# Performance work log

Measured on AMD Instinct MI355X. Metric: run time of the kernel, lower is better.

## Reference

```python
import jax, jax.numpy as jnp
import numpy as np

N = 100000   # nodes
E = 1600000  # edges
D = 128      # feature dim
DO = 3       # out_head target dim
C = 50000    # centers


def setup_inputs() -> dict:
    key = jax.random.key(0)
    k1, k2, k3, k4 = jax.random.split(key, 4)
    H = jax.random.normal(k1, (N, D), dtype=jnp.float32)
    W = jax.random.normal(k2, (D, DO), dtype=jnp.float32) / np.sqrt(D)
    b = jnp.zeros((DO,), dtype=jnp.float32)
    target = jax.random.normal(k3, (N, DO), dtype=jnp.float32)
    edge_index = jax.random.randint(k4, (2, E), 0, N, dtype=jnp.int32)
    centers = jnp.arange(C, dtype=jnp.int32)  # distinct center node ids
    return {"H": H, "W": W, "b": b, "target": target,
            "edge_index": edge_index, "centers": centers}


def reference(H, W, b, target, edge_index, centers):
    # Vectorized equivalent of the per-center Python loop:
    # for each edge (s, d): if s is a center, pair (owner(s), d) contributes
    # mean-squared error of out_head(H[d]) vs target[d]; then per-center mean,
    # then mean over all centers (empty centers contribute 0 via cnt clamp).
    n_nodes = H.shape[0]
    n_centers = centers.shape[0]
    # node id -> center slot (n_centers == "not a center" sentinel)
    owner_of = jnp.full((n_nodes,), n_centers, dtype=jnp.int32)
    owner_of = owner_of.at[centers].set(jnp.arange(n_centers, dtype=jnp.int32))
    src, dst = edge_index[0], edge_index[1]
    owners = owner_of[src]              # [E]
    mask = owners < n_centers           # [E] edge rooted at a center

    z_frontier = H[dst]                 # [E, D] neighbor-feature gather
    y_hat = z_frontier @ W + b          # [E, DO] out_head (linear)
    y_true = target[dst]                # [E, DO]
    err = jnp.mean((y_hat - y_true) ** 2, axis=-1)  # [E]
    errm = jnp.where(mask, err, jnp.zeros((), err.dtype))

    # segment-mean per center; sentinel bucket n_centers dropped
    loss_sum = jax.ops.segment_sum(errm, owners, num_segments=n_centers + 1)[:n_centers]
    cnt = jax.ops.segment_sum(mask.astype(err.dtype), owners,
                              num_segments=n_centers + 1)[:n_centers]
    aux_loss = jnp.mean(loss_sum / jnp.maximum(cnt, 1.0))
    return aux_loss
```

## Files before the change

kernel.cpp:

```cpp
#include <hip/hip_runtime.h>


#define CNT_SHIFT 44
#define ERR_SCALE 67108864.0f
#define BKT_SHIFT 8
#define BKT_SIZE  256
#define P2B       256
#define ERRB      512
#define BTHR      512
#define STASH     6272
#define PREF_STRIDE 200

__device__ __forceinline__ int owner_fn(int s, bool fast, int C,
                                        const int* __restrict__ arr_idx,
                                        const int* __restrict__ centers) {
    if (fast) return (s < C) ? s : -1;
    int i = arr_idx[s];
    return ((unsigned)i < (unsigned)C && centers[i] == s) ? i : -1;
}

__global__ __launch_bounds__(256)
void prep_kernel(const int* __restrict__ centers,
                 int* __restrict__ arr_idx,
                 int* __restrict__ flagpart,
                 float* __restrict__ out,
                 int C, int out_size) {
    __shared__ int ok;
    int t = threadIdx.x;
    int gtid = blockIdx.x * 256 + t;
    if (t == 0) ok = 1;
    __syncthreads();
    bool mism = false;
    if (gtid < C) {
        int c = centers[gtid];
        arr_idx[c] = gtid;
        mism = (c != gtid);
    }
    if (__ballot(mism) != 0ull && (t & 63) == 0) atomicAnd(&ok, 0);
    __syncthreads();
    if (t == 0) flagpart[blockIdx.x] = ok;
    if (gtid >= 1 && gtid < out_size) out[gtid] = 0.f;
}

__global__ __launch_bounds__(BTHR)
void mid_kernel(const float* __restrict__ H, const float* __restrict__ W,
                const float* __restrict__ b, const float* __restrict__ target,
                const int* __restrict__ eidx, const int* __restrict__ centers,
                const int* __restrict__ arr_idx,
                const int* __restrict__ flagpart,
                float* __restrict__ err_node,
                unsigned short* __restrict__ pref_g,
                unsigned int* __restrict__ pairs,
                int N, int E, int C, int NB, int NBV) {
    __shared__ unsigned int stash[STASH];
    __shared__ unsigned int hist[256];
    __shared__ unsigned int scan[256];
    __shared__ unsigned int total_sh;
    __shared__ int okf;
    const int t = threadIdx.x;

    if (blockIdx.x < P2B) {
        if (t == 0) okf = 1;
        if (t < 256) hist[t] = 0u;
        __syncthreads();
        bool my_ok = (t < NBV) ? (flagpart[t] != 0) : true;
        if (__ballot(!my_ok) != 0ull && (t & 63) == 0) atomicAnd(&okf, 0);
        __syncthreads();
        const bool fast = (okf != 0);

        const int E4     = E >> 2;
        const int chunk4 = (E4 + P2B - 1) / P2B;
        const int c0     = blockIdx.x * chunk4;
        const int c1     = min(E4, c0 + chunk4);
        const int4* r0 = reinterpret_cast<const int4*>(eidx);
        const int4* r1 = reinterpret_cast<const int4*>(eidx + E);

        for (int i = c0 + t; i < c1; i += BTHR) {
            int4 s4 = r0[i];
            int ss[4] = {s4.x, s4.y, s4.z, s4.w};
            #pragma unroll
            for (int k = 0; k < 4; ++k) {
                int o = owner_fn(ss[k], fast, C, arr_idx, centers);
                if (o >= 0) atomicAdd(&hist[(unsigned)o >> BKT_SHIFT], 1u);
            }
        }
        __syncthreads();
        if (t < 256) scan[t] = hist[t];
        __syncthreads();
        for (int off = 1; off < 256; off <<= 1) {
            unsigned v = (t < 256 && t >= off) ? scan[t - off] : 0u;
            __syncthreads();
            if (t < 256 && t >= off) scan[t] += v;
            __syncthreads();
        }
        if (t < 256) {
            unsigned pre = (t == 0) ? 0u : scan[t - 1];
            hist[t] = pre;
            if (t <= NB)
                pref_g[(size_t)blockIdx.x * PREF_STRIDE + t] = (unsigned short)pre;
        }
        if (t == 0) total_sh = scan[255];
        __syncthreads();
        for (int i = c0 + t; i < c1; i += BTHR) {
            int4 s4 = r0[i];
            int4 d4 = r1[i];
            int ss[4] = {s4.x, s4.y, s4.z, s4.w};
            int dd[4] = {d4.x, d4.y, d4.z, d4.w};
            #pragma unroll
            for (int k = 0; k < 4; ++k) {
                int o = owner_fn(ss[k], fast, C, arr_idx, centers);
                if (o >= 0) {
                    unsigned bk = (unsigned)o >> BKT_SHIFT;
                    unsigned pos = atomicAdd(&hist[bk], 1u);
                    stash[pos] = (((unsigned)o & (BKT_SIZE - 1)) << 17)
                               | (unsigned)dd[k];
                }
            }
        }
        __syncthreads();
        {
            unsigned nvec = (total_sh + 3u) >> 2;
            uint4*       dg = reinterpret_cast<uint4*>(pairs + (size_t)blockIdx.x * STASH);
            const uint4* sg = reinterpret_cast<const uint4*>(stash);
            for (unsigned i = t; i < nvec; i += BTHR) dg[i] = sg[i];
        }
    } else {
        const int lane = t & 63, sub = lane >> 5, l32 = lane & 31;
        float wr[12];
        {
            const float* wb = W + (size_t)(4 * l32) * 3;
            #pragma unroll
            for (int r = 0; r < 12; ++r) wr[r] = wb[r];
        }
        const float b0 = b[0], b1 = b[1], b2 = b[2];
        const float4* H4 = reinterpret_cast<const float4*>(H);
        const int wv    = (blockIdx.x - P2B) * (BTHR >> 6) + (t >> 6);
        const int EW    = ERRB * (BTHR >> 6);
        const int npair = (N + 1) >> 1;
        for (int p = wv; p < npair; p += EW) {
            const int node = 2 * p + sub;
            float4 hv = (node < N) ? H4[(size_t)node * 32 + l32]
                                   : make_float4(0.f, 0.f, 0.f, 0.f);
            float hx[4] = {hv.x, hv.y, hv.z, hv.w};
            float a0 = 0.f, a1 = 0.f, a2 = 0.f;
            #pragma unroll
            for (int r = 0; r < 4; ++r) {
                a0 += hx[r] * wr[r * 3 + 0];
                a1 += hx[r] * wr[r * 3 + 1];
                a2 += hx[r] * wr[r * 3 + 2];
            }
            #pragma unroll
            for (int m = 16; m > 0; m >>= 1) {
                a0 += __shfl_xor(a0, m, 64);
                a1 += __shfl_xor(a1, m, 64);
                a2 += __shfl_xor(a2, m, 64);
            }
            if (l32 == 0 && node < N) {
                float e0 = a0 + b0 - target[(size_t)node * 3 + 0];
                float e1 = a1 + b1 - target[(size_t)node * 3 + 1];
                float e2 = a2 + b2 - target[(size_t)node * 3 + 2];
                err_node[node] = (e0*e0 + e1*e1 + e2*e2) * (1.0f / 3.0f);
            }
        }
    }
}

__global__ __launch_bounds__(1024)
void reduce_kernel(const unsigned int* __restrict__ pairs,
                   const unsigned short* __restrict__ pref_g,
                   const float* __restrict__ err_node,
                   float* __restrict__ partial, int C) {
    __shared__ unsigned long long bins[BKT_SIZE];
    __shared__ float wsum[16];
    const int bk = blockIdx.x, t = threadIdx.x;
    if (t < BKT_SIZE) bins[t] = 0ull;
    __syncthreads();
    {
        const int seg = t >> 2;
        const int j   = t & 3;
        const size_t pb = (size_t)seg * PREF_STRIDE;
        unsigned start = pref_g[pb + bk];
        unsigned end   = pref_g[pb + bk + 1];
        const unsigned int* reg = pairs + (size_t)seg * STASH;
        for (unsigned i = start + j; i < end; i += 4) {
            unsigned p = reg[i];
            float err = err_node[p & 0x1FFFFu];
            atomicAdd(&bins[p >> 17],
                      (1ull << CNT_SHIFT) + (unsigned long long)(err * ERR_SCALE));
        }
    }
    __syncthreads();
    float term = 0.f;
    if (t < BKT_SIZE) {
        int center = bk * BKT_SIZE + t;
        if (center < C) {
            unsigned long long u = bins[t];
            float cnt = (float)(u >> CNT_SHIFT);
            float es  = (float)(u & ((1ull << CNT_SHIFT) - 1)) * (1.0f / ERR_SCALE);
            term = es / fmaxf(cnt, 1.0f);
        }
    }
    #pragma unroll
    for (int m = 32; m > 0; m >>= 1) term += __shfl_down(term, m, 64);
    if ((t & 63) == 0) wsum[t >> 6] = term;
    __syncthreads();
    if (t == 0) {
        float s = 0.f;
        #pragma unroll
        for (int w = 0; w < 16; ++w) s += wsum[w];
        partial[bk] = s;
    }
}

__global__ __launch_bounds__(256)
void final_kernel(const float* __restrict__ partial,
                  float* __restrict__ out, int NB, float invC) {
    __shared__ float wsum[4];
    const int t = threadIdx.x;
    float v = (t < NB) ? partial[t] : 0.f;
    #pragma unroll
    for (int m = 32; m > 0; m >>= 1) v += __shfl_down(v, m, 64);
    if ((t & 63) == 0) wsum[t >> 6] = v;
    __syncthreads();
    if (t == 0) out[0] = (wsum[0] + wsum[1] + wsum[2] + wsum[3]) * invC;
}

__global__ __launch_bounds__(256)
void fb_err_kernel(const float* __restrict__ H, const float* __restrict__ W,
                   const float* __restrict__ b, const float* __restrict__ target,
                   const int* __restrict__ centers,
                   float* __restrict__ err_node, int* __restrict__ arr_idx,
                   float* __restrict__ out, int N, int C, int D, int DO,
                   int out_size) {
    int gtid = blockIdx.x * blockDim.x + threadIdx.x;
    if (gtid < C) arr_idx[centers[gtid]] = gtid;
    if (gtid < out_size) out[gtid] = 0.f;
    if (gtid < N) {
        float acc = 0.f;
        for (int j = 0; j < DO; ++j) {
            float a = b[j];
            for (int r = 0; r < D; ++r)
                a += H[(size_t)gtid * D + r] * W[(size_t)r * DO + j];
            float e = a - target[(size_t)gtid * DO + j];
            acc += e * e;
        }
        err_node[gtid] = acc / (float)DO;
    }
}

__global__ void fb_edge_kernel(const int* __restrict__ eidx,
                               const int* __restrict__ arr_idx,
                               const int* __restrict__ centers,
                               const float* __restrict__ err_node,
                               unsigned long long* __restrict__ binsg,
                               int E, int C) {
    int e = blockIdx.x * blockDim.x + threadIdx.x;
    if (e >= E) return;
    int s = eidx[e];
    int o = owner_fn(s, false, C, arr_idx, centers);
    if (o >= 0) {
        int d = eidx[E + e];
        unsigned long long add = (1ull << CNT_SHIFT)
                               + (unsigned long long)(err_node[d] * ERR_SCALE);
        atomicAdd(&binsg[o], add);
    }
}

__global__ void fb_finalize_kernel(const unsigned long long* __restrict__ binsg,
                                   float* __restrict__ out, int C) {
    int i = blockIdx.x * blockDim.x + threadIdx.x;
    float term = 0.f;
    if (i < C) {
        unsigned long long u = binsg[i];
        float cnt = (float)(u >> CNT_SHIFT);
        float es  = (float)(u & ((1ull << CNT_SHIFT) - 1)) * (1.0f / ERR_SCALE);
        term = es / fmaxf(cnt, 1.0f);
    }
    #pragma unroll
    for (int m = 32; m > 0; m >>= 1) term += __shfl_down(term, m, 64);
    __shared__ float wsum[4];
    if ((threadIdx.x & 63) == 0) wsum[threadIdx.x >> 6] = term;
    __syncthreads();
    if (threadIdx.x == 0)
        atomicAdd(out, (wsum[0] + wsum[1] + wsum[2] + wsum[3]) / (float)C);
}

extern "C" void kernel_launch(void* const* d_in, const int* in_sizes, int n_in,
                              void* d_out, int out_size, void* d_ws, size_t ws_size,
                              hipStream_t stream) {
    const float* H      = (const float*)d_in[0];
    const float* W      = (const float*)d_in[1];
    const float* b      = (const float*)d_in[2];
    const float* target = (const float*)d_in[3];
    const int*   eidx   = (const int*)d_in[4];
    const int*   ctrs   = (const int*)d_in[5];

    const int DO = in_sizes[2];
    const int D  = in_sizes[1] / DO;
    const int N  = in_sizes[0] / D;
    const int E  = in_sizes[4] / 2;
    const int C  = in_sizes[5];
    const int NB  = (C + BKT_SIZE - 1) >> BKT_SHIFT;
    const int NBV = (C + 255) / 256;

    size_t off = 0;
    auto take = [&](size_t bytes) {
        void* p = (char*)d_ws + off;
        off = (off + bytes + 255) & ~255ull;
        return p;
    };
    float*          err_node = (float*)take((size_t)N * 4);
    int*            arr_idx  = (int*)take((size_t)N * 4);
    int*            flagpart = (int*)take((size_t)NBV * 4);
    unsigned short* pref_g   = (unsigned short*)take((size_t)P2B * PREF_STRIDE * 2);
    float*          partial  = (float*)take((size_t)NB * 4);
    unsigned int*   pairs    = (unsigned int*)((char*)d_ws + off);
    size_t need = off + (size_t)P2B * STASH * 4;

    int chunk_edges = 4 * ((E / 4 + P2B - 1) / P2B);
    bool fits = (ws_size >= need) && (NB + 1 <= PREF_STRIDE) && (NBV <= BTHR) &&
                (N < (1 << 17)) && ((E & 3) == 0) && (chunk_edges <= STASH) &&
                (D == 128) && (DO == 3) && (out_size >= 1);
    if (fits) {
        prep_kernel<<<NBV, 256, 0, stream>>>(ctrs, arr_idx, flagpart,
                                             (float*)d_out, C, out_size);
        mid_kernel<<<P2B + ERRB, BTHR, 0, stream>>>(H, W, b, target, eidx,
                                                    ctrs, arr_idx, flagpart,
                                                    err_node, pref_g, pairs,
                                                    N, E, C, NB, NBV);
        reduce_kernel<<<NB, 1024, 0, stream>>>(pairs, pref_g, err_node,
                                               partial, C);
        final_kernel<<<1, 256, 0, stream>>>(partial, (float*)d_out, NB,
                                            1.0f / (float)C);
    } else {
        unsigned long long* binsg = (unsigned long long*)((char*)d_ws + off);
        hipMemsetAsync(binsg, 0, (size_t)C * 8, stream);
        int thr = 256;
        fb_err_kernel<<<(max(N, C) + thr - 1) / thr, thr, 0, stream>>>(
            H, W, b, target, ctrs, err_node, arr_idx, (float*)d_out,
            N, C, D, DO, out_size);
        fb_edge_kernel<<<(E + thr - 1) / thr, thr, 0, stream>>>(
            eidx, arr_idx, ctrs, err_node, binsg, E, C);
        fb_finalize_kernel<<<(C + thr - 1) / thr, thr, 0, stream>>>(
            binsg, (float*)d_out, C);
    }
}
```

Baseline: 35.16 us.

## Move per-node error into prep kernel and split bucketize into its own kernel

```diff
diff --git a/kernel.cpp b/kernel.cpp
--- a/kernel.cpp
+++ b/kernel.cpp
@@ -6,8 +6,8 @@
 #define BKT_SHIFT 8
 #define BKT_SIZE  256
 #define P2B       256
-#define ERRB      512
-#define BTHR      512
+#define BKT_THR   1024
+#define ERRBLKS   2048
 #define STASH     6272
 #define PREF_STRIDE 200
 
@@ -20,38 +20,80 @@
 }
 
 __global__ __launch_bounds__(256)
-void prep_kernel(const int* __restrict__ centers,
-                 int* __restrict__ arr_idx,
-                 int* __restrict__ flagpart,
-                 float* __restrict__ out,
-                 int C, int out_size) {
+void prep_err_kernel(const float* __restrict__ H, const float* __restrict__ W,
+                     const float* __restrict__ b, const float* __restrict__ target,
+                     const int* __restrict__ centers,
+                     float* __restrict__ err_node,
+                     int* __restrict__ arr_idx,
+                     int* __restrict__ flagpart,
+                     float* __restrict__ out,
+                     int N, int C, int NBV, int out_size) {
     __shared__ int ok;
-    int t = threadIdx.x;
-    int gtid = blockIdx.x * 256 + t;
-    if (t == 0) ok = 1;
-    __syncthreads();
-    bool mism = false;
-    if (gtid < C) {
-        int c = centers[gtid];
-        arr_idx[c] = gtid;
-        mism = (c != gtid);
-    }
-    if (__ballot(mism) != 0ull && (t & 63) == 0) atomicAnd(&ok, 0);
-    __syncthreads();
-    if (t == 0) flagpart[blockIdx.x] = ok;
+    const int t = threadIdx.x;
+    const int gtid = blockIdx.x * 256 + t;
+
+    if (blockIdx.x < NBV) {
+        if (t == 0) ok = 1;
+        __syncthreads();
+        bool mism = false;
+        if (gtid < C) {
+            int c = centers[gtid];
+            arr_idx[c] = gtid;
+            mism = (c != gtid);
+        }
+        if (__ballot(mism) != 0ull && (t & 63) == 0) atomicAnd(&ok, 0);
+        __syncthreads();
+        if (t == 0) flagpart[blockIdx.x] = ok;
+    }
     if (gtid >= 1 && gtid < out_size) out[gtid] = 0.f;
-}
-
-__global__ __launch_bounds__(BTHR)
-void mid_kernel(const float* __restrict__ H, const float* __restrict__ W,
-                const float* __restrict__ b, const float* __restrict__ target,
-                const int* __restrict__ eidx, const int* __restrict__ centers,
-                const int* __restrict__ arr_idx,
-                const int* __restrict__ flagpart,
-                float* __restrict__ err_node,
-                unsigned short* __restrict__ pref_g,
-                unsigned int* __restrict__ pairs,
-                int N, int E, int C, int NB, int NBV) {
+
+    const int lane = t & 63, sub = lane >> 5, l32 = lane & 31;
+    float wr[12];
+    {
+        const float* wb = W + (size_t)(4 * l32) * 3;
+        #pragma unroll
+        for (int r = 0; r < 12; ++r) wr[r] = wb[r];
+    }
+    const float b0 = b[0], b1 = b[1], b2 = b[2];
+    const float4* H4 = reinterpret_cast<const float4*>(H);
+    const int wv    = blockIdx.x * 4 + (t >> 6);
+    const int EW    = ERRBLKS * 4;
+    const int npair = (N + 1) >> 1;
+    for (int p = wv; p < npair; p += EW) {
+        const int node = 2 * p + sub;
+        float4 hv = (node < N) ? H4[(size_t)node * 32 + l32]
+                               : make_float4(0.f, 0.f, 0.f, 0.f);
+        float hx[4] = {hv.x, hv.y, hv.z, hv.w};
+        float a0 = 0.f, a1 = 0.f, a2 = 0.f;
+        #pragma unroll
+        for (int r = 0; r < 4; ++r) {
+            a0 += hx[r] * wr[r * 3 + 0];
+            a1 += hx[r] * wr[r * 3 + 1];
+            a2 += hx[r] * wr[r * 3 + 2];
+        }
+        #pragma unroll
+        for (int m = 16; m > 0; m >>= 1) {
+            a0 += __shfl_xor(a0, m, 64);
+            a1 += __shfl_xor(a1, m, 64);
+            a2 += __shfl_xor(a2, m, 64);
+        }
+        if (l32 == 0 && node < N) {
+            float e0 = a0 + b0 - target[(size_t)node * 3 + 0];
+            float e1 = a1 + b1 - target[(size_t)node * 3 + 1];
+            float e2 = a2 + b2 - target[(size_t)node * 3 + 2];
+            err_node[node] = (e0*e0 + e1*e1 + e2*e2) * (1.0f / 3.0f);
+        }
+    }
+}
+
+__global__ __launch_bounds__(BKT_THR)
+void bucketize_kernel(const int* __restrict__ eidx,
+                      const int* __restrict__ centers,
+                      const int* __restrict__ arr_idx,
+                      const int* __restrict__ flagpart,
+                      unsigned short* __restrict__ pref_g,
+                      unsigned int* __restrict__ pairs,
+                      int E, int C, int NB, int NBV) {
     __shared__ unsigned int stash[STASH];
     __shared__ unsigned int hist[256];
     __shared__ unsigned int scan[256];
@@ -59,109 +101,69 @@
     __shared__ int okf;
     const int t = threadIdx.x;
 
-    if (blockIdx.x < P2B) {
-        if (t == 0) okf = 1;
-        if (t < 256) hist[t] = 0u;
+    if (t == 0) okf = 1;
+    if (t < 256) hist[t] = 0u;
+    __syncthreads();
+    bool my_ok = (t < NBV) ? (flagpart[t] != 0) : true;
+    if (__ballot(!my_ok) != 0ull && (t & 63) == 0) atomicAnd(&okf, 0);
+    __syncthreads();
+    const bool fast = (okf != 0);
+
+    const int E4     = E >> 2;
+    const int chunk4 = (E4 + P2B - 1) / P2B;
+    const int c0     = blockIdx.x * chunk4;
+    const int c1     = min(E4, c0 + chunk4);
+    const int4* r0 = reinterpret_cast<const int4*>(eidx);
+    const int4* r1 = reinterpret_cast<const int4*>(eidx + E);
+
+    for (int i = c0 + t; i < c1; i += BKT_THR) {
+        int4 s4 = r0[i];
+        int ss[4] = {s4.x, s4.y, s4.z, s4.w};
+        #pragma unroll
+        for (int k = 0; k < 4; ++k) {
+            int o = owner_fn(ss[k], fast, C, arr_idx, centers);
+            if (o >= 0) atomicAdd(&hist[(unsigned)o >> BKT_SHIFT], 1u);
+        }
+    }
+    __syncthreads();
+    if (t < 256) scan[t] = hist[t];
+    __syncthreads();
+    for (int off = 1; off < 256; off <<= 1) {
+        unsigned v = (t < 256 && t >= off) ? scan[t - off] : 0u;
         __syncthreads();
-        bool my_ok = (t < NBV) ? (flagpart[t] != 0) : true;
-        if (__ballot(!my_ok) != 0ull && (t & 63) == 0) atomicAnd(&okf, 0);
+        if (t < 256 && t >= off) scan[t] += v;
         __syncthreads();
-        const bool fast = (okf != 0);
-
-        const int E4     = E >> 2;
-        const int chunk4 = (E4 + P2B - 1) / P2B;
-        const int c0     = blockIdx.x * chunk4;
-        const int c1     = min(E4, c0 + chunk4);
-        const int4* r0 = reinterpret_cast<const int4*>(eidx);
-        const int4* r1 = reinterpret_cast<const int4*>(eidx + E);
-
-        for (int i = c0 + t; i < c1; i += BTHR) {
-            int4 s4 = r0[i];
-            int ss[4] = {s4.x, s4.y, s4.z, s4.w};
-            #pragma unroll
-            for (int k = 0; k < 4; ++k) {
-                int o = owner_fn(ss[k], fast, C, arr_idx, centers);
-                if (o >= 0) atomicAdd(&hist[(unsigned)o >> BKT_SHIFT], 1u);
+    }
+    if (t < 256) {
+        unsigned pre = (t == 0) ? 0u : scan[t - 1];
+        hist[t] = pre;
+        if (t <= NB)
+            pref_g[(size_t)blockIdx.x * PREF_STRIDE + t] = (unsigned short)pre;
+    }
+    if (t == 0) total_sh = scan[255];
+    __syncthreads();
+    for (int i = c0 + t; i < c1; i += BKT_THR) {
+        int4 s4 = r0[i];
+        int4 d4 = r1[i];
+        int ss[4] = {s4.x, s4.y, s4.z, s4.w};
+        int dd[4] = {d4.x, d4.y, d4.z, d4.w};
+        #pragma unroll
+        for (int k = 0; k < 4; ++k) {
+            int o = owner_fn(ss[k], fast, C, arr_idx, centers);
+            if (o >= 0) {
+                unsigned bk = (unsigned)o >> BKT_SHIFT;
+                unsigned pos = atomicAdd(&hist[bk], 1u);
+                stash[pos] = (((unsigned)o & (BKT_SIZE - 1)) << 17)
+                           | (unsigned)dd[k];
             }
         }
-        __syncthreads();
-        if (t < 256) scan[t] = hist[t];
-        __syncthreads();
-        for (int off = 1; off < 256; off <<= 1) {
-            unsigned v = (t < 256 && t >= off) ? scan[t - off] : 0u;
-            __syncthreads();
-            if (t < 256 && t >= off) scan[t] += v;
-            __syncthreads();
-        }
-        if (t < 256) {
-            unsigned pre = (t == 0) ? 0u : scan[t - 1];
-            hist[t] = pre;
-            if (t <= NB)
-                pref_g[(size_t)blockIdx.x * PREF_STRIDE + t] = (unsigned short)pre;
-        }
-        if (t == 0) total_sh = scan[255];
-        __syncthreads();
-        for (int i = c0 + t; i < c1; i += BTHR) {
-            int4 s4 = r0[i];
-            int4 d4 = r1[i];
-            int ss[4] = {s4.x, s4.y, s4.z, s4.w};
-            int dd[4] = {d4.x, d4.y, d4.z, d4.w};
-            #pragma unroll
-            for (int k = 0; k < 4; ++k) {
-                int o = owner_fn(ss[k], fast, C, arr_idx, centers);
-                if (o >= 0) {
-                    unsigned bk = (unsigned)o >> BKT_SHIFT;
-                    unsigned pos = atomicAdd(&hist[bk], 1u);
-                    stash[pos] = (((unsigned)o & (BKT_SIZE - 1)) << 17)
-                               | (unsigned)dd[k];
-                }
-            }
-        }
-        __syncthreads();
-        {
-            unsigned nvec = (total_sh + 3u) >> 2;
-            uint4*       dg = reinterpret_cast<uint4*>(pairs + (size_t)blockIdx.x * STASH);
-            const uint4* sg = reinterpret_cast<const uint4*>(stash);
-            for (unsigned i = t; i < nvec; i += BTHR) dg[i] = sg[i];
-        }
-    } else {
-        const int lane = t & 63, sub = lane >> 5, l32 = lane & 31;
-        float wr[12];
-        {
-            const float* wb = W + (size_t)(4 * l32) * 3;
-            #pragma unroll
-            for (int r = 0; r < 12; ++r) wr[r] = wb[r];
-        }
-        const float b0 = b[0], b1 = b[1], b2 = b[2];
-        const float4* H4 = reinterpret_cast<const float4*>(H);
-        const int wv    = (blockIdx.x - P2B) * (BTHR >> 6) + (t >> 6);
-        const int EW    = ERRB * (BTHR >> 6);
-        const int npair = (N + 1) >> 1;
-        for (int p = wv; p < npair; p += EW) {
-            const int node = 2 * p + sub;
-            float4 hv = (node < N) ? H4[(size_t)node * 32 + l32]
-                                   : make_float4(0.f, 0.f, 0.f, 0.f);
-            float hx[4] = {hv.x, hv.y, hv.z, hv.w};
-            float a0 = 0.f, a1 = 0.f, a2 = 0.f;
-            #pragma unroll
-            for (int r = 0; r < 4; ++r) {
-                a0 += hx[r] * wr[r * 3 + 0];
-                a1 += hx[r] * wr[r * 3 + 1];
-                a2 += hx[r] * wr[r * 3 + 2];
-            }
-            #pragma unroll
-            for (int m = 16; m > 0; m >>= 1) {
-                a0 += __shfl_xor(a0, m, 64);
-                a1 += __shfl_xor(a1, m, 64);
-                a2 += __shfl_xor(a2, m, 64);
-            }
-            if (l32 == 0 && node < N) {
-                float e0 = a0 + b0 - target[(size_t)node * 3 + 0];
-                float e1 = a1 + b1 - target[(size_t)node * 3 + 1];
-                float e2 = a2 + b2 - target[(size_t)node * 3 + 2];
-                err_node[node] = (e0*e0 + e1*e1 + e2*e2) * (1.0f / 3.0f);
-            }
-        }
+    }
+    __syncthreads();
+    {
+        unsigned nvec = (total_sh + 3u) >> 2;
+        uint4*       dg = reinterpret_cast<uint4*>(pairs + (size_t)blockIdx.x * STASH);
+        const uint4* sg = reinterpret_cast<const uint4*>(stash);
+        for (unsigned i = t; i < nvec; i += BKT_THR) dg[i] = sg[i];
     }
 }
 
@@ -318,16 +320,17 @@
     size_t need = off + (size_t)P2B * STASH * 4;
 
     int chunk_edges = 4 * ((E / 4 + P2B - 1) / P2B);
-    bool fits = (ws_size >= need) && (NB + 1 <= PREF_STRIDE) && (NBV <= BTHR) &&
-                (N < (1 << 17)) && ((E & 3) == 0) && (chunk_edges <= STASH) &&
-                (D == 128) && (DO == 3) && (out_size >= 1);
+    bool fits = (ws_size >= need) && (NB + 1 <= PREF_STRIDE) && (NBV <= BKT_THR) &&
+                (NBV <= ERRBLKS) && (N < (1 << 17)) && ((E & 3) == 0) &&
+                (chunk_edges <= STASH) && (D == 128) && (DO == 3) && (out_size >= 1);
     if (fits) {
-        prep_kernel<<<NBV, 256, 0, stream>>>(ctrs, arr_idx, flagpart,
-                                             (float*)d_out, C, out_size);
-        mid_kernel<<<P2B + ERRB, BTHR, 0, stream>>>(H, W, b, target, eidx,
-                                                    ctrs, arr_idx, flagpart,
-                                                    err_node, pref_g, pairs,
-                                                    N, E, C, NB, NBV);
+        prep_err_kernel<<<ERRBLKS, 256, 0, stream>>>(H, W, b, target, ctrs,
+                                                     err_node, arr_idx, flagpart,
+                                                     (float*)d_out, N, C, NBV,
+                                                     out_size);
+        bucketize_kernel<<<P2B, BKT_THR, 0, stream>>>(eidx, ctrs, arr_idx,
+                                                      flagpart, pref_g, pairs,
+                                                      E, C, NB, NBV);
         reduce_kernel<<<NB, 1024, 0, stream>>>(pairs, pref_g, err_node,
                                                partial, C);
         final_kernel<<<1, 256, 0, stream>>>(partial, (float*)d_out, NB,
```

New measurement: 34.87 us. Within noise of the previous version (-0.8%).
